# Optimization experiments

Hardware: AMD Instinct MI355X
Metric: run time of the kernel (lower is better)

Reference implementation:

```python
import jax, jax.numpy as jnp
import numpy as np

EPS = 1e-6
NUM_HEADS = 16

def _ln(x):
    # LayerNorm32, no affine, eps=1e-6, computed in fp32
    x32 = x.astype(jnp.float32)
    mu = jnp.mean(x32, axis=-1, keepdims=True)
    var = jnp.var(x32, axis=-1, keepdims=True)
    return ((x32 - mu) * jax.lax.rsqrt(var + EPS)).astype(x.dtype)

def _mha(q, k, v):
    # q,k,v: [B, L, H, D]
    d = q.shape[-1]
    scale = 1.0 / jnp.sqrt(jnp.asarray(d, q.dtype))
    s = jnp.einsum('bqhd,bkhd->bhqk', q, k) * scale
    p = jax.nn.softmax(s, axis=-1)
    o = jnp.einsum('bhqk,bkhd->bqhd', p, v)
    return o.reshape(o.shape[0], o.shape[1], -1)

def setup_inputs() -> dict:
    key = jax.random.key(0)
    ks = jax.random.split(key, 10)
    B, L, C, Lc, Cc = 4, 2048, 1024, 1024, 1024
    Dff = 4 * C
    s = 0.02
    return {
        'x': jax.random.normal(ks[0], (B, L, C), jnp.float32),
        'context': jax.random.normal(ks[1], (B, Lc, Cc), jnp.float32),
        'w_qkv': jax.random.normal(ks[2], (C, 3 * C), jnp.float32) * s,
        'b_qkv': jnp.zeros((3 * C,), jnp.float32),
        'w_os': jax.random.normal(ks[3], (C, C), jnp.float32) * s,
        'b_os': jnp.zeros((C,), jnp.float32),
        'w_qc': jax.random.normal(ks[4], (C, C), jnp.float32) * s,
        'b_qc': jnp.zeros((C,), jnp.float32),
        'w_kvc': jax.random.normal(ks[5], (Cc, 2 * C), jnp.float32) * s,
        'b_kvc': jnp.zeros((2 * C,), jnp.float32),
        'w_oc': jax.random.normal(ks[6], (C, C), jnp.float32) * s,
        'b_oc': jnp.zeros((C,), jnp.float32),
        'w_fc1': jax.random.normal(ks[7], (C, Dff), jnp.float32) * s,
        'b_fc1': jnp.zeros((Dff,), jnp.float32),
        'w_fc2': jax.random.normal(ks[8], (Dff, C), jnp.float32) * s,
        'b_fc2': jnp.zeros((C,), jnp.float32),
    }

def reference(x, context, w_qkv, b_qkv, w_os, b_os, w_qc, b_qc, w_kvc, b_kvc,
              w_oc, b_oc, w_fc1, b_fc1, w_fc2, b_fc2):
    B, L, C = x.shape
    H = NUM_HEADS
    D = C // H
    # --- self attention (pre-norm, full) ---
    h = _ln(x)
    qkv = (h @ w_qkv + b_qkv).reshape(B, L, 3, H, D)
    q, k, v = qkv[:, :, 0], qkv[:, :, 1], qkv[:, :, 2]
    h = _mha(q, k, v) @ w_os + b_os
    x = x + h
    # --- cross attention ---
    h = _ln(x)
    q = (h @ w_qc + b_qc).reshape(B, L, H, D)
    Lc = context.shape[1]
    kv = (context @ w_kvc + b_kvc).reshape(B, Lc, 2, H, D)
    k, v = kv[:, :, 0], kv[:, :, 1]
    h = _mha(q, k, v) @ w_oc + b_oc
    x = x + h
    # --- sparse FFN (GELU tanh) ---
    h = _ln(x)
    h = jax.nn.gelu(h @ w_fc1 + b_fc1, approximate=True) @ w_fc2 + b_fc2
    return x + h
```

## Files before the change

kernel.cpp:

```cpp
#include <hip/hip_runtime.h>

typedef unsigned short ushort_t;
typedef __attribute__((ext_vector_type(8))) short short8;
typedef __attribute__((ext_vector_type(4))) float f32x4;
typedef __attribute__((ext_vector_type(4))) unsigned short ushort4v;

__device__ inline ushort_t f2bf(float f) {
    union { float f; unsigned u; } v; v.f = f;
    return (ushort_t)((v.u + 0x7FFFu + ((v.u >> 16) & 1u)) >> 16);
}
__device__ inline float bf2f(ushort_t u) {
    union { unsigned u; float f; } v; v.u = ((unsigned)u) << 16;
    return v.f;
}

__device__ inline void gld16(const ushort_t* g, ushort_t* l) {
    __builtin_amdgcn_global_load_lds(
        (const __attribute__((address_space(1))) unsigned int*)g,
        (__attribute__((address_space(3))) unsigned int*)l, 16, 0, 0);
}

__device__ inline int xcd_swz(int id, int nwg) {
    int q = nwg >> 3;
    return (id & 7) * q + (id >> 3);
}

__global__ void w_transpose_bf16(const float* __restrict__ w, ushort_t* __restrict__ out,
                                 int K, int N) {
    __shared__ float t[64][65];
    const int k0 = blockIdx.y * 64, n0 = blockIdx.x * 64;
    const int tid = threadIdx.x;
#pragma unroll
    for (int i = 0; i < 16; i++) {
        int idx = tid + i * 256;
        int r = idx >> 6, c = idx & 63;
        t[r][c] = w[(size_t)(k0 + r) * N + n0 + c];
    }
    __syncthreads();
#pragma unroll
    for (int i = 0; i < 16; i++) {
        int idx = tid + i * 256;
        int nr = idx >> 6, kc = idx & 63;
        out[(size_t)(n0 + nr) * K + k0 + kc] = f2bf(t[kc][nr]);
    }
}

__global__ void v_transpose(const ushort_t* __restrict__ V, int vStride, int rowsPerBatch,
                            ushort_t* __restrict__ Vt, int Lk) {
    __shared__ __align__(16) ushort_t t[64][72];
    const int bh = blockIdx.y, k0 = blockIdx.x * 64;
    const int b = bh >> 4, h = bh & 15;
    const int tid = threadIdx.x;
    const ushort_t* src = V + (size_t)(b * rowsPerBatch + k0) * vStride + h * 64;
#pragma unroll
    for (int i = 0; i < 2; i++) {
        int ch = tid + i * 256;
        int r = ch >> 3, c = (ch & 7) * 8;
        *(short8*)(&t[r][c]) = *(const short8*)(src + (size_t)r * vStride + c);
    }
    __syncthreads();
#pragma unroll
    for (int i = 0; i < 2; i++) {
        int ch = tid + i * 256;
        int d = ch >> 3, c = (ch & 7) * 8;
        short8 o;
#pragma unroll
        for (int j = 0; j < 8; j++) o[j] = (short)t[c + j][d];
        *(short8*)(Vt + ((size_t)bh * 64 + d) * Lk + k0 + c) = o;
    }
}

__global__ void f32_to_bf16_vec(const float* __restrict__ in, ushort_t* __restrict__ out, int n4) {
    int i = blockIdx.x * blockDim.x + threadIdx.x;
    if (i < n4) {
        float4 v = ((const float4*)in)[i];
        ushort4v o;
        o[0] = f2bf(v.x); o[1] = f2bf(v.y); o[2] = f2bf(v.z); o[3] = f2bf(v.w);
        ((ushort4v*)out)[i] = o;
    }
}

__global__ void ln_rows(const float* __restrict__ in, ushort_t* __restrict__ out) {
    __shared__ float s1[4], s2[4];
    const int row = blockIdx.x;
    const int tid = threadIdx.x;
    const float4 v = ((const float4*)(in + (size_t)row * 1024))[tid];
    float s  = v.x + v.y + v.z + v.w;
    float ss = v.x * v.x + v.y * v.y + v.z * v.z + v.w * v.w;
#pragma unroll
    for (int d = 32; d >= 1; d >>= 1) {
        s  += __shfl_down(s, d, 64);
        ss += __shfl_down(ss, d, 64);
    }
    if ((tid & 63) == 0) { s1[tid >> 6] = s; s2[tid >> 6] = ss; }
    __syncthreads();
    float sum = s1[0] + s1[1] + s1[2] + s1[3];
    float sqs = s2[0] + s2[1] + s2[2] + s2[3];
    float mu  = sum * (1.0f / 1024.0f);
    float var = sqs * (1.0f / 1024.0f) - mu * mu;
    float rs  = rsqrtf(var + 1e-6f);
    ushort4v o;
    o[0] = f2bf((v.x - mu) * rs);
    o[1] = f2bf((v.y - mu) * rs);
    o[2] = f2bf((v.z - mu) * rs);
    o[3] = f2bf((v.w - mu) * rs);
    ((ushort4v*)(out + (size_t)row * 1024))[tid] = o;
}

#define EPI_BF16 0
#define EPI_GELU 1
#define EPI_RES  2

template <int EPI>
__global__ void gemm_bt(const ushort_t* __restrict__ A, const ushort_t* __restrict__ Bt,
                        const float* __restrict__ bias, const float* __restrict__ res,
                        void* __restrict__ outp, int M, int N, int K) {
    __shared__ __align__(16) ushort_t As[128 * 64];
    __shared__ __align__(16) ushort_t Bs[128 * 64];
    const int tid = threadIdx.x;
    const int lane = tid & 63, wave = tid >> 6;
    const int nwg = gridDim.x * gridDim.y;
    const int sid = xcd_swz(blockIdx.y * gridDim.x + blockIdx.x, nwg);
    const int m0 = (sid / gridDim.x) * 128, n0 = (sid % gridDim.x) * 128;
    const int wr = (wave >> 1) * 64, wc = (wave & 1) * 64;
    const int lr = lane & 15, lg = lane >> 4;

    f32x4 acc[4][4];
#pragma unroll
    for (int i = 0; i < 4; i++)
#pragma unroll
        for (int j = 0; j < 4; j++) acc[i][j] = f32x4{0.f, 0.f, 0.f, 0.f};

    for (int k0 = 0; k0 < K; k0 += 64) {
#pragma unroll
        for (int i = 0; i < 4; i++) {
            int ch = tid + i * 256;
            int r = ch >> 3;
            int kcs = (((ch & 7) ^ (r & 7))) * 8;
            gld16(A  + (size_t)(m0 + r) * K + k0 + kcs, As + ch * 8);
            gld16(Bt + (size_t)(n0 + r) * K + k0 + kcs, Bs + ch * 8);
        }
        __syncthreads();
#pragma unroll
        for (int ks = 0; ks < 2; ks++) {
            short8 af[4], bfr[4];
#pragma unroll
            for (int m = 0; m < 4; m++) {
                int r = wr + m * 16 + lr;
                int kc = ks * 4 + lg;
                af[m] = *(const short8*)(As + r * 64 + ((kc ^ (r & 7)) << 3));
            }
#pragma unroll
            for (int n = 0; n < 4; n++) {
                int r = wc + n * 16 + lr;
                int kc = ks * 4 + lg;
                bfr[n] = *(const short8*)(Bs + r * 64 + ((kc ^ (r & 7)) << 3));
            }
#pragma unroll
            for (int m = 0; m < 4; m++)
#pragma unroll
                for (int n = 0; n < 4; n++)
                    acc[m][n] = __builtin_amdgcn_mfma_f32_16x16x32_bf16(af[m], bfr[n], acc[m][n], 0, 0, 0);
        }
        __syncthreads();
    }

#pragma unroll
    for (int m = 0; m < 4; m++) {
        int rowb = m0 + wr + m * 16 + lg * 4;
#pragma unroll
        for (int n = 0; n < 4; n++) {
            int col = n0 + wc + n * 16 + lr;
            float bcol = bias[col];
            f32x4 v = acc[m][n];
#pragma unroll
            for (int q = 0; q < 4; q++) {
                float x = v[q] + bcol;
                if (EPI == EPI_GELU) {
                    float u = 0.7978845608028654f * (x + 0.044715f * x * x * x);
                    x = 0.5f * x * (1.0f + tanhf(u));
                }
                size_t off = (size_t)(rowb + q) * N + col;
                if (EPI == EPI_RES) ((float*)outp)[off] = x + res[off];
                else                ((ushort_t*)outp)[off] = f2bf(x);
            }
        }
    }
}

__global__ __launch_bounds__(512, 2)
void attn_fwd(const ushort_t* __restrict__ Q, int qStride,
              const ushort_t* __restrict__ Kp, int kvStride, int kvBatchRows,
              const ushort_t* __restrict__ Vt, int Lk,
              ushort_t* __restrict__ O) {
    __shared__ __align__(16) ushort_t Ks[2][64 * 64];
    __shared__ __align__(16) ushort_t Vts[2][64 * 64];
    __shared__ __align__(16) ushort_t Ps[8][16 * 64];
    const int tid = threadIdx.x, lane = tid & 63, wave = tid >> 6;
    const int lr = lane & 15, lg = lane >> 4;
    const int sid = xcd_swz(blockIdx.x, gridDim.x);
    const int qb = sid & 15, h = (sid >> 4) & 15, b = sid >> 8;
    const int qRow0 = b * 2048 + qb * 128;
    const int kvRow0 = b * kvBatchRows;
    const int hc = h * 64;
    const ushort_t* vt_base = Vt + (size_t)(b * 16 + h) * 64 * Lk;

    short8 qf[2];
    {
        const ushort_t* qrow = Q + (size_t)(qRow0 + wave * 16 + lr) * qStride + hc;
        short8 r0 = *(const short8*)(qrow + lg * 8);
        short8 r1 = *(const short8*)(qrow + 32 + lg * 8);
#pragma unroll
        for (int j = 0; j < 8; j++) {
            qf[0][j] = (short)f2bf(bf2f((ushort_t)r0[j]) * 0.125f);
            qf[1][j] = (short)f2bf(bf2f((ushort_t)r1[j]) * 0.125f);
        }
    }

    f32x4 oacc[4];
#pragma unroll
    for (int d = 0; d < 4; d++) oacc[d] = f32x4{0.f, 0.f, 0.f, 0.f};
    float mrun = -INFINITY, lrun = 0.f;

    const int nt = Lk >> 6;

    auto stage = [&](int buf, int kt) {
        int r = tid >> 3;
        int kcs = (((tid & 7) ^ (r & 7))) * 8;
        gld16(Kp + (size_t)(kvRow0 + kt + r) * kvStride + hc + kcs, Ks[buf] + tid * 8);
        gld16(vt_base + (size_t)r * Lk + kt + kcs, Vts[buf] + tid * 8);
    };

    stage(0, 0);
    __syncthreads();
    int cur = 0;

    for (int t = 0; t < nt; ++t) {
        if (t + 1 < nt) stage(cur ^ 1, (t + 1) * 64);

        const ushort_t* Kc = Ks[cur];
        const ushort_t* Vc = Vts[cur];

        f32x4 sacc[4];
        __builtin_amdgcn_s_setprio(1);
#pragma unroll
        for (int n = 0; n < 4; n++) {
            int r = n * 16 + lr;
            short8 k0 = *(const short8*)(Kc + r * 64 + ((lg ^ (r & 7)) << 3));
            short8 k1 = *(const short8*)(Kc + r * 64 + (((4 + lg) ^ (r & 7)) << 3));
            f32x4 s = f32x4{0.f, 0.f, 0.f, 0.f};
            s = __builtin_amdgcn_mfma_f32_16x16x32_bf16(k0, qf[0], s, 0, 0, 0);
            s = __builtin_amdgcn_mfma_f32_16x16x32_bf16(k1, qf[1], s, 0, 0, 0);
            sacc[n] = s;
        }
        __builtin_amdgcn_s_setprio(0);

        float mx = sacc[0][0];
#pragma unroll
        for (int n = 0; n < 4; n++)
#pragma unroll
            for (int r = 0; r < 4; r++) if (n | r) mx = fmaxf(mx, sacc[n][r]);
        mx = fmaxf(mx, __shfl_xor(mx, 16, 64));
        mx = fmaxf(mx, __shfl_xor(mx, 32, 64));

        if (!__all(mx <= mrun + 8.0f)) {
            float mnew = fmaxf(mrun, mx);
            float al = __expf(mrun - mnew);
            float a0 = __shfl(al, lg * 4 + 0, 64);
            float a1 = __shfl(al, lg * 4 + 1, 64);
            float a2 = __shfl(al, lg * 4 + 2, 64);
            float a3 = __shfl(al, lg * 4 + 3, 64);
#pragma unroll
            for (int dn = 0; dn < 4; dn++) {
                oacc[dn][0] *= a0; oacc[dn][1] *= a1;
                oacc[dn][2] *= a2; oacc[dn][3] *= a3;
            }
            lrun *= al;
            mrun = mnew;
        }

        float rsum = 0.f;
#pragma unroll
        for (int n = 0; n < 4; n++)
#pragma unroll
            for (int r = 0; r < 4; r++) {
                float p = __expf(sacc[n][r] - mrun);
                sacc[n][r] = p;
                rsum += p;
            }
        rsum += __shfl_xor(rsum, 16, 64);
        rsum += __shfl_xor(rsum, 32, 64);
        lrun += rsum;

        ushort_t* Pw = &Ps[wave][0];
#pragma unroll
        for (int n = 0; n < 4; n++) {
            unsigned w0, w1;
            asm("v_cvt_pk_bf16_f32 %0, %1, %2" : "=v"(w0) : "v"(sacc[n][0]), "v"(sacc[n][1]));
            asm("v_cvt_pk_bf16_f32 %0, %1, %2" : "=v"(w1) : "v"(sacc[n][2]), "v"(sacc[n][3]));
            int kc = n * 2 + (lg >> 1);
            uint2 u; u.x = w0; u.y = w1;
            *(uint2*)((char*)Pw + lr * 128 + ((kc ^ (lr & 7)) << 4) + (lg & 1) * 8) = u;
        }

        short8 pf0 = *(const short8*)(Pw + lr * 64 + ((lg ^ (lr & 7)) << 3));
        short8 pf1 = *(const short8*)(Pw + lr * 64 + (((4 + lg) ^ (lr & 7)) << 3));
        __builtin_amdgcn_s_setprio(1);
#pragma unroll
        for (int dn = 0; dn < 4; dn++) {
            int r = dn * 16 + lr;
            short8 v0 = *(const short8*)(Vc + r * 64 + ((lg ^ (r & 7)) << 3));
            short8 v1 = *(const short8*)(Vc + r * 64 + (((4 + lg) ^ (r & 7)) << 3));
            oacc[dn] = __builtin_amdgcn_mfma_f32_16x16x32_bf16(pf0, v0, oacc[dn], 0, 0, 0);
            oacc[dn] = __builtin_amdgcn_mfma_f32_16x16x32_bf16(pf1, v1, oacc[dn], 0, 0, 0);
        }
        __builtin_amdgcn_s_setprio(0);
        __syncthreads();
        cur ^= 1;
    }

    float linv[4];
#pragma unroll
    for (int r = 0; r < 4; r++) linv[r] = 1.0f / __shfl(lrun, lg * 4 + r, 64);

#pragma unroll
    for (int dn = 0; dn < 4; dn++)
#pragma unroll
        for (int q = 0; q < 4; q++) {
            float o = oacc[dn][q] * linv[q];
            int row = qRow0 + wave * 16 + lg * 4 + q;
            int col = hc + dn * 16 + lr;
            O[(size_t)row * 1024 + col] = f2bf(o);
        }
}

extern "C" void kernel_launch(void* const* d_in, const int* in_sizes, int n_in,
                              void* d_out, int out_size, void* d_ws, size_t ws_size,
                              hipStream_t stream) {
    const float* x     = (const float*)d_in[0];
    const float* ctx   = (const float*)d_in[1];
    const float* w_qkv = (const float*)d_in[2];
    const float* b_qkv = (const float*)d_in[3];
    const float* w_os  = (const float*)d_in[4];
    const float* b_os  = (const float*)d_in[5];
    const float* w_qc  = (const float*)d_in[6];
    const float* b_qc  = (const float*)d_in[7];
    const float* w_kvc = (const float*)d_in[8];
    const float* b_kvc = (const float*)d_in[9];
    const float* w_oc  = (const float*)d_in[10];
    const float* b_oc  = (const float*)d_in[11];
    const float* w_fc1 = (const float*)d_in[12];
    const float* b_fc1 = (const float*)d_in[13];
    const float* w_fc2 = (const float*)d_in[14];
    const float* b_fc2 = (const float*)d_in[15];
    float* out = (float*)d_out;

    char* ws = (char*)d_ws;
    ushort_t* wqkvT = (ushort_t*)(ws + 0);
    ushort_t* wosT  = (ushort_t*)(ws + 6291456);
    ushort_t* wqcT  = (ushort_t*)(ws + 8388608);
    ushort_t* wkvcT = (ushort_t*)(ws + 10485760);
    ushort_t* wocT  = (ushort_t*)(ws + 14680064);
    ushort_t* wfc1T = (ushort_t*)(ws + 16777216);
    ushort_t* wfc2T = (ushort_t*)(ws + 25165824);
    ushort_t* qkv_bf  = (ushort_t*)(ws + 33554432);
    ushort_t* q_bf    = (ushort_t*)(ws + 33554432);
    ushort_t* kv_bf   = (ushort_t*)(ws + 50331648);
    ushort_t* vt_c    = (ushort_t*)(ws + 67108864);
    ushort_t* ffn_bf  = (ushort_t*)(ws + 33554432);
    ushort_t* ctx_bf  = (ushort_t*)(ws + 83886080);
    ushort_t* attn_bf = (ushort_t*)(ws + 92274688);
    ushort_t* h_bf    = (ushort_t*)(ws + 109051904);
    ushort_t* vt_s    = (ushort_t*)(ws + 109051904);

    const dim3 tb(256);
    const dim3 tb512(512);
    w_transpose_bf16<<<dim3(48, 16), tb, 0, stream>>>(w_qkv, wqkvT, 1024, 3072);
    w_transpose_bf16<<<dim3(16, 16), tb, 0, stream>>>(w_os,  wosT,  1024, 1024);
    w_transpose_bf16<<<dim3(16, 16), tb, 0, stream>>>(w_qc,  wqcT,  1024, 1024);
    w_transpose_bf16<<<dim3(32, 16), tb, 0, stream>>>(w_kvc, wkvcT, 1024, 2048);
    w_transpose_bf16<<<dim3(16, 16), tb, 0, stream>>>(w_oc,  wocT,  1024, 1024);
    w_transpose_bf16<<<dim3(64, 16), tb, 0, stream>>>(w_fc1, wfc1T, 1024, 4096);
    w_transpose_bf16<<<dim3(16, 64), tb, 0, stream>>>(w_fc2, wfc2T, 4096, 1024);
    f32_to_bf16_vec<<<4096, tb, 0, stream>>>(ctx, ctx_bf, 1048576);

    ln_rows<<<8192, tb, 0, stream>>>(x, h_bf);
    gemm_bt<EPI_BF16><<<dim3(24, 64), tb, 0, stream>>>(h_bf, wqkvT, b_qkv, nullptr, qkv_bf, 8192, 3072, 1024);
    v_transpose<<<dim3(32, 64), tb, 0, stream>>>(qkv_bf + 2048, 3072, 2048, vt_s, 2048);
    attn_fwd<<<dim3(1024), tb512, 0, stream>>>(qkv_bf, 3072, qkv_bf + 1024, 3072, 2048,
                                               vt_s, 2048, attn_bf);
    gemm_bt<EPI_RES><<<dim3(8, 64), tb, 0, stream>>>(attn_bf, wosT, b_os, x, out, 8192, 1024, 1024);

    ln_rows<<<8192, tb, 0, stream>>>(out, h_bf);
    gemm_bt<EPI_BF16><<<dim3(8, 64), tb, 0, stream>>>(h_bf, wqcT, b_qc, nullptr, q_bf, 8192, 1024, 1024);
    gemm_bt<EPI_BF16><<<dim3(16, 32), tb, 0, stream>>>(ctx_bf, wkvcT, b_kvc, nullptr, kv_bf, 4096, 2048, 1024);
    v_transpose<<<dim3(16, 64), tb, 0, stream>>>(kv_bf + 1024, 2048, 1024, vt_c, 1024);
    attn_fwd<<<dim3(1024), tb512, 0, stream>>>(q_bf, 1024, kv_bf, 2048, 1024,
                                               vt_c, 1024, attn_bf);
    gemm_bt<EPI_RES><<<dim3(8, 64), tb, 0, stream>>>(attn_bf, wocT, b_oc, out, out, 8192, 1024, 1024);

    ln_rows<<<8192, tb, 0, stream>>>(out, h_bf);
    gemm_bt<EPI_GELU><<<dim3(32, 64), tb, 0, stream>>>(h_bf, wfc1T, b_fc1, nullptr, ffn_bf, 8192, 4096, 1024);
    gemm_bt<EPI_RES><<<dim3(8, 64), tb, 0, stream>>>(ffn_bf, wfc2T, b_fc2, out, out, 8192, 1024, 4096);
}
```

Baseline: 589.6 us.

## Rework attention to 32x32x16 MFMA with register P exchange and exp2 softmax

The attention kernel moves from 16x16x32 MFMA tiles with 8 waves of 16 query rows to 32x32x16 MFMA tiles with 4 waves of 32 query rows each. Each lane now holds a full query row, so the row max and sum need only one cross-lane shuffle. The P tile is passed to the PV MFMA through a lane-xor-32 shuffle in registers instead of an LDS round trip, and softmax uses exp2 with log2(e) folded into the Q scale, with the running max preloaded into the S accumulators. Block size drops to 256 threads with a launch bound of 3 blocks per CU. The larger tiles use more registers per lane, which may limit occupancy, and the loads per tile are split into two passes.

New measurement: 600.7 us. No clear change (+1.9%).

```diff
diff --git a/kernel.cpp b/kernel.cpp
--- a/kernel.cpp
+++ b/kernel.cpp
@@ -3,6 +3,7 @@
 typedef unsigned short ushort_t;
 typedef __attribute__((ext_vector_type(8))) short short8;
 typedef __attribute__((ext_vector_type(4))) float f32x4;
+typedef __attribute__((ext_vector_type(16))) float f32x16;
 typedef __attribute__((ext_vector_type(4))) unsigned short ushort4v;
 
 __device__ inline ushort_t f2bf(float f) {
@@ -188,47 +189,52 @@
     }
 }
 
-__global__ __launch_bounds__(512, 2)
+__global__ __launch_bounds__(256, 3)
 void attn_fwd(const ushort_t* __restrict__ Q, int qStride,
               const ushort_t* __restrict__ Kp, int kvStride, int kvBatchRows,
               const ushort_t* __restrict__ Vt, int Lk,
               ushort_t* __restrict__ O) {
     __shared__ __align__(16) ushort_t Ks[2][64 * 64];
     __shared__ __align__(16) ushort_t Vts[2][64 * 64];
-    __shared__ __align__(16) ushort_t Ps[8][16 * 64];
     const int tid = threadIdx.x, lane = tid & 63, wave = tid >> 6;
-    const int lr = lane & 15, lg = lane >> 4;
+    const int ql = lane & 31;
+    const int hh = lane >> 5;
     const int sid = xcd_swz(blockIdx.x, gridDim.x);
-    const int qb = sid & 15, h = (sid >> 4) & 15, b = sid >> 8;
+    const int qb = sid & 15, hd = (sid >> 4) & 15, b = sid >> 8;
     const int qRow0 = b * 2048 + qb * 128;
     const int kvRow0 = b * kvBatchRows;
-    const int hc = h * 64;
-    const ushort_t* vt_base = Vt + (size_t)(b * 16 + h) * 64 * Lk;
-
-    short8 qf[2];
+    const int hc = hd * 64;
+    const ushort_t* vt_base = Vt + (size_t)(b * 16 + hd) * 64 * Lk;
+
+    short8 qf[4];
     {
-        const ushort_t* qrow = Q + (size_t)(qRow0 + wave * 16 + lr) * qStride + hc;
-        short8 r0 = *(const short8*)(qrow + lg * 8);
-        short8 r1 = *(const short8*)(qrow + 32 + lg * 8);
-#pragma unroll
-        for (int j = 0; j < 8; j++) {
-            qf[0][j] = (short)f2bf(bf2f((ushort_t)r0[j]) * 0.125f);
-            qf[1][j] = (short)f2bf(bf2f((ushort_t)r1[j]) * 0.125f);
-        }
-    }
-
-    f32x4 oacc[4];
-#pragma unroll
-    for (int d = 0; d < 4; d++) oacc[d] = f32x4{0.f, 0.f, 0.f, 0.f};
-    float mrun = -INFINITY, lrun = 0.f;
+        const ushort_t* qrow = Q + (size_t)(qRow0 + wave * 32 + ql) * qStride + hc + hh * 8;
+        const float s = 0.125f * 1.44269504088896f;
+#pragma unroll
+        for (int mi = 0; mi < 4; mi++) {
+            short8 r = *(const short8*)(qrow + mi * 16);
+#pragma unroll
+            for (int j = 0; j < 8; j++) qf[mi][j] = (short)f2bf(bf2f((ushort_t)r[j]) * s);
+        }
+    }
+
+    f32x16 o0, o1;
+#pragma unroll
+    for (int r = 0; r < 16; r++) { o0[r] = 0.f; o1[r] = 0.f; }
+    float mrun = 0.f, lrun = 0.f;
 
     const int nt = Lk >> 6;
+    const int sw = ql & 7;
 
     auto stage = [&](int buf, int kt) {
-        int r = tid >> 3;
-        int kcs = (((tid & 7) ^ (r & 7))) * 8;
-        gld16(Kp + (size_t)(kvRow0 + kt + r) * kvStride + hc + kcs, Ks[buf] + tid * 8);
-        gld16(vt_base + (size_t)r * Lk + kt + kcs, Vts[buf] + tid * 8);
+#pragma unroll
+        for (int i = 0; i < 2; i++) {
+            int ch = tid + i * 256;
+            int r = ch >> 3;
+            int kcs = (((ch & 7) ^ (r & 7))) * 8;
+            gld16(Kp + (size_t)(kvRow0 + kt + r) * kvStride + hc + kcs, Ks[buf] + ch * 8);
+            gld16(vt_base + (size_t)r * Lk + kt + kcs, Vts[buf] + ch * 8);
+        }
     };
 
     stage(0, 0);
@@ -241,97 +247,91 @@
         const ushort_t* Kc = Ks[cur];
         const ushort_t* Vc = Vts[cur];
 
-        f32x4 sacc[4];
+        f32x16 s0, s1;
+#pragma unroll
+        for (int r = 0; r < 16; r++) { s0[r] = -mrun; s1[r] = -mrun; }
         __builtin_amdgcn_s_setprio(1);
 #pragma unroll
-        for (int n = 0; n < 4; n++) {
-            int r = n * 16 + lr;
-            short8 k0 = *(const short8*)(Kc + r * 64 + ((lg ^ (r & 7)) << 3));
-            short8 k1 = *(const short8*)(Kc + r * 64 + (((4 + lg) ^ (r & 7)) << 3));
-            f32x4 s = f32x4{0.f, 0.f, 0.f, 0.f};
-            s = __builtin_amdgcn_mfma_f32_16x16x32_bf16(k0, qf[0], s, 0, 0, 0);
-            s = __builtin_amdgcn_mfma_f32_16x16x32_bf16(k1, qf[1], s, 0, 0, 0);
-            sacc[n] = s;
+        for (int mi = 0; mi < 4; mi++) {
+            short8 a0 = *(const short8*)(Kc + ql * 64 + (((2 * mi + hh) ^ sw) << 3));
+            short8 a1 = *(const short8*)(Kc + (32 + ql) * 64 + (((2 * mi + hh) ^ sw) << 3));
+            s0 = __builtin_amdgcn_mfma_f32_32x32x16_bf16(a0, qf[mi], s0, 0, 0, 0);
+            s1 = __builtin_amdgcn_mfma_f32_32x32x16_bf16(a1, qf[mi], s1, 0, 0, 0);
         }
         __builtin_amdgcn_s_setprio(0);
 
-        float mx = sacc[0][0];
-#pragma unroll
-        for (int n = 0; n < 4; n++)
-#pragma unroll
-            for (int r = 0; r < 4; r++) if (n | r) mx = fmaxf(mx, sacc[n][r]);
-        mx = fmaxf(mx, __shfl_xor(mx, 16, 64));
+        float mx = fmaxf(s0[0], s0[1]);
+#pragma unroll
+        for (int r = 2; r < 16; r++) mx = fmaxf(mx, s0[r]);
+#pragma unroll
+        for (int r = 0; r < 16; r++) mx = fmaxf(mx, s1[r]);
         mx = fmaxf(mx, __shfl_xor(mx, 32, 64));
 
-        if (!__all(mx <= mrun + 8.0f)) {
-            float mnew = fmaxf(mrun, mx);
-            float al = __expf(mrun - mnew);
-            float a0 = __shfl(al, lg * 4 + 0, 64);
-            float a1 = __shfl(al, lg * 4 + 1, 64);
-            float a2 = __shfl(al, lg * 4 + 2, 64);
-            float a3 = __shfl(al, lg * 4 + 3, 64);
-#pragma unroll
-            for (int dn = 0; dn < 4; dn++) {
-                oacc[dn][0] *= a0; oacc[dn][1] *= a1;
-                oacc[dn][2] *= a2; oacc[dn][3] *= a3;
-            }
+        if (!__all(mx <= 8.0f)) {
+            float d = fmaxf(mx, 0.0f);
+            float al = exp2f(-d);
+#pragma unroll
+            for (int r = 0; r < 16; r++) { o0[r] *= al; o1[r] *= al; }
             lrun *= al;
-            mrun = mnew;
+            mrun += d;
+#pragma unroll
+            for (int r = 0; r < 16; r++) { s0[r] -= d; s1[r] -= d; }
         }
 
         float rsum = 0.f;
 #pragma unroll
-        for (int n = 0; n < 4; n++)
-#pragma unroll
-            for (int r = 0; r < 4; r++) {
-                float p = __expf(sacc[n][r] - mrun);
-                sacc[n][r] = p;
-                rsum += p;
-            }
-        rsum += __shfl_xor(rsum, 16, 64);
+        for (int r = 0; r < 16; r++) { s0[r] = exp2f(s0[r]); rsum += s0[r]; }
+#pragma unroll
+        for (int r = 0; r < 16; r++) { s1[r] = exp2f(s1[r]); rsum += s1[r]; }
         rsum += __shfl_xor(rsum, 32, 64);
         lrun += rsum;
 
-        ushort_t* Pw = &Ps[wave][0];
-#pragma unroll
-        for (int n = 0; n < 4; n++) {
-            unsigned w0, w1;
-            asm("v_cvt_pk_bf16_f32 %0, %1, %2" : "=v"(w0) : "v"(sacc[n][0]), "v"(sacc[n][1]));
-            asm("v_cvt_pk_bf16_f32 %0, %1, %2" : "=v"(w1) : "v"(sacc[n][2]), "v"(sacc[n][3]));
-            int kc = n * 2 + (lg >> 1);
-            uint2 u; u.x = w0; u.y = w1;
-            *(uint2*)((char*)Pw + lr * 128 + ((kc ^ (lr & 7)) << 4) + (lg & 1) * 8) = u;
-        }
-
-        short8 pf0 = *(const short8*)(Pw + lr * 64 + ((lg ^ (lr & 7)) << 3));
-        short8 pf1 = *(const short8*)(Pw + lr * 64 + (((4 + lg) ^ (lr & 7)) << 3));
+        unsigned W0[8], W1[8];
+#pragma unroll
+        for (int g = 0; g < 4; g++) {
+            asm("v_cvt_pk_bf16_f32 %0, %1, %2" : "=v"(W0[g * 2 + 0]) : "v"(s0[4 * g + 0]), "v"(s0[4 * g + 1]));
+            asm("v_cvt_pk_bf16_f32 %0, %1, %2" : "=v"(W0[g * 2 + 1]) : "v"(s0[4 * g + 2]), "v"(s0[4 * g + 3]));
+            asm("v_cvt_pk_bf16_f32 %0, %1, %2" : "=v"(W1[g * 2 + 0]) : "v"(s1[4 * g + 0]), "v"(s1[4 * g + 1]));
+            asm("v_cvt_pk_bf16_f32 %0, %1, %2" : "=v"(W1[g * 2 + 1]) : "v"(s1[4 * g + 2]), "v"(s1[4 * g + 3]));
+        }
+
         __builtin_amdgcn_s_setprio(1);
 #pragma unroll
-        for (int dn = 0; dn < 4; dn++) {
-            int r = dn * 16 + lr;
-            short8 v0 = *(const short8*)(Vc + r * 64 + ((lg ^ (r & 7)) << 3));
-            short8 v1 = *(const short8*)(Vc + r * 64 + (((4 + lg) ^ (r & 7)) << 3));
-            oacc[dn] = __builtin_amdgcn_mfma_f32_16x16x32_bf16(pf0, v0, oacc[dn], 0, 0, 0);
-            oacc[dn] = __builtin_amdgcn_mfma_f32_16x16x32_bf16(pf1, v1, oacc[dn], 0, 0, 0);
+        for (int w = 0; w < 4; w++) {
+            const int p2 = (w & 1) * 2;
+            union { unsigned u[4]; short8 s8; } pf;
+#pragma unroll
+            for (int i = 0; i < 2; i++) {
+                unsigned A0 = (w >> 1) ? W1[p2 * 2 + i] : W0[p2 * 2 + i];
+                unsigned A1 = (w >> 1) ? W1[(p2 + 1) * 2 + i] : W0[(p2 + 1) * 2 + i];
+                unsigned own  = hh ? A1 : A0;
+                unsigned send = hh ? A0 : A1;
+                unsigned recv = __shfl_xor(send, 32, 64);
+                pf.u[0 + i] = hh ? recv : own;
+                pf.u[2 + i] = hh ? own : recv;
+            }
+            short8 v0 = *(const short8*)(Vc + ql * 64 + (((2 * w + hh) ^ sw) << 3));
+            short8 v1 = *(const short8*)(Vc + (32 + ql) * 64 + (((2 * w + hh) ^ sw) << 3));
+            o0 = __builtin_amdgcn_mfma_f32_32x32x16_bf16(v0, pf.s8, o0, 0, 0, 0);
+            o1 = __builtin_amdgcn_mfma_f32_32x32x16_bf16(v1, pf.s8, o1, 0, 0, 0);
         }
         __builtin_amdgcn_s_setprio(0);
         __syncthreads();
         cur ^= 1;
     }
 
-    float linv[4];
-#pragma unroll
-    for (int r = 0; r < 4; r++) linv[r] = 1.0f / __shfl(lrun, lg * 4 + r, 64);
-
-#pragma unroll
-    for (int dn = 0; dn < 4; dn++)
-#pragma unroll
-        for (int q = 0; q < 4; q++) {
-            float o = oacc[dn][q] * linv[q];
-            int row = qRow0 + wave * 16 + lg * 4 + q;
-            int col = hc + dn * 16 + lr;
-            O[(size_t)row * 1024 + col] = f2bf(o);
-        }
+    float linv = 1.0f / lrun;
+    ushort_t* orow = O + (size_t)(qRow0 + wave * 32 + ql) * 1024 + hc + 4 * hh;
+#pragma unroll
+    for (int g = 0; g < 4; g++) {
+        ushort4v ov;
+#pragma unroll
+        for (int j = 0; j < 4; j++) ov[j] = f2bf(o0[4 * g + j] * linv);
+        *(ushort4v*)(orow + 8 * g) = ov;
+#pragma unroll
+        for (int j = 0; j < 4; j++) ov[j] = f2bf(o1[4 * g + j] * linv);
+        *(ushort4v*)(orow + 32 + 8 * g) = ov;
+    }
 }
 
 extern "C" void kernel_launch(void* const* d_in, const int* in_sizes, int n_in,
@@ -374,7 +374,6 @@
     ushort_t* vt_s    = (ushort_t*)(ws + 109051904);
 
     const dim3 tb(256);
-    const dim3 tb512(512);
     w_transpose_bf16<<<dim3(48, 16), tb, 0, stream>>>(w_qkv, wqkvT, 1024, 3072);
     w_transpose_bf16<<<dim3(16, 16), tb, 0, stream>>>(w_os,  wosT,  1024, 1024);
     w_transpose_bf16<<<dim3(16, 16), tb, 0, stream>>>(w_qc,  wqcT,  1024, 1024);
@@ -387,16 +386,16 @@
     ln_rows<<<8192, tb, 0, stream>>>(x, h_bf);
     gemm_bt<EPI_BF16><<<dim3(24, 64), tb, 0, stream>>>(h_bf, wqkvT, b_qkv, nullptr, qkv_bf, 8192, 3072, 1024);
     v_transpose<<<dim3(32, 64), tb, 0, stream>>>(qkv_bf + 2048, 3072, 2048, vt_s, 2048);
-    attn_fwd<<<dim3(1024), tb512, 0, stream>>>(qkv_bf, 3072, qkv_bf + 1024, 3072, 2048,
-                                               vt_s, 2048, attn_bf);
+    attn_fwd<<<dim3(1024), tb, 0, stream>>>(qkv_bf, 3072, qkv_bf + 1024, 3072, 2048,
+                                            vt_s, 2048, attn_bf);
     gemm_bt<EPI_RES><<<dim3(8, 64), tb, 0, stream>>>(attn_bf, wosT, b_os, x, out, 8192, 1024, 1024);
 
     ln_rows<<<8192, tb, 0, stream>>>(out, h_bf);
     gemm_bt<EPI_BF16><<<dim3(8, 64), tb, 0, stream>>>(h_bf, wqcT, b_qc, nullptr, q_bf, 8192, 1024, 1024);
     gemm_bt<EPI_BF16><<<dim3(16, 32), tb, 0, stream>>>(ctx_bf, wkvcT, b_kvc, nullptr, kv_bf, 4096, 2048, 1024);
     v_transpose<<<dim3(16, 64), tb, 0, stream>>>(kv_bf + 1024, 2048, 1024, vt_c, 1024);
-    attn_fwd<<<dim3(1024), tb512, 0, stream>>>(q_bf, 1024, kv_bf, 2048, 1024,
-                                               vt_c, 1024, attn_bf);
+    attn_fwd<<<dim3(1024), tb, 0, stream>>>(q_bf, 1024, kv_bf, 2048, 1024,
+                                            vt_c, 1024, attn_bf);
     gemm_bt<EPI_RES><<<dim3(8, 64), tb, 0, stream>>>(attn_bf, wocT, b_oc, out, out, 8192, 1024, 1024);
 
     ln_rows<<<8192, tb, 0, stream>>>(out, h_bf);
```

## Add 256x256-tile GEMM with phased prefetch for QKV and FC1 projections

Applied to the files above, without the earlier changes.

Adds a new GEMM kernel with 256x256 output tiles, 512 threads and a double-buffered LDS pipeline. Global loads for the next k-tiles are interleaved across four MFMA phases, with explicit waitcnt and barriers between them. It replaces the 128-tile GEMM for the two widest projections (QKV and FC1) to raise arithmetic intensity and cut global traffic per FLOP. The cost is much higher register and LDS use (128 KB of shared buffers), fewer blocks in the grid, and hand-tuned vmcnt counts that must match the issued loads.

New measurement: 611.4 us. +3.7%, slower.

```diff
diff --git a/kernel.cpp b/kernel.cpp
--- a/kernel.cpp
+++ b/kernel.cpp
@@ -183,6 +183,128 @@
                 size_t off = (size_t)(rowb + q) * N + col;
                 if (EPI == EPI_RES) ((float*)outp)[off] = x + res[off];
                 else                ((ushort_t*)outp)[off] = f2bf(x);
+            }
+        }
+    }
+}
+
+template <int EPI>
+__global__ __launch_bounds__(512, 2)
+void gemm256_bt(const ushort_t* __restrict__ A, const ushort_t* __restrict__ Bt,
+                const float* __restrict__ bias,
+                void* __restrict__ outp, int M, int N, int K) {
+    __shared__ __align__(16) ushort_t As[2][256 * 64];
+    __shared__ __align__(16) ushort_t Bs[2][256 * 64];
+    const int tid = threadIdx.x;
+    const int lane = tid & 63, wave = tid >> 6;
+    const int wm = wave >> 2, wn = wave & 3;
+    const int lr = lane & 15, lg = lane >> 4;
+    const int ntx = gridDim.x;
+    const int sid = xcd_swz(blockIdx.y * ntx + blockIdx.x, ntx * gridDim.y);
+    const int m0 = (sid / ntx) * 256, n0 = (sid % ntx) * 256;
+    const int nkt = K >> 6;
+
+    f32x4 acc[8][4];
+#pragma unroll
+    for (int i = 0; i < 8; i++)
+#pragma unroll
+        for (int j = 0; j < 4; j++) acc[i][j] = f32x4{0.f, 0.f, 0.f, 0.f};
+
+    auto stageAQ = [&](int slot, int kt, int q) {
+        int r_ = (tid >> 8) * 128 + q * 32 + ((tid >> 3) & 31);
+        int c_ = tid & 7;
+        gld16(A + (size_t)(m0 + r_) * K + kt + ((c_ ^ (r_ & 7)) << 3),
+              &As[slot][r_ * 64 + c_ * 8]);
+    };
+    auto stageBH = [&](int slot, int kt, int h) {
+#pragma unroll
+        for (int i = 0; i < 2; i++) {
+            int ch = tid + i * 512;
+            int r_ = h * 128 + (ch >> 3);
+            int c_ = ch & 7;
+            gld16(Bt + (size_t)(n0 + r_) * K + kt + ((c_ ^ (r_ & 7)) << 3),
+                  &Bs[slot][r_ * 64 + c_ * 8]);
+        }
+    };
+
+#define RD_A(slot, mf, ks)                                                      \
+    (*(const short8*)(&As[slot][(wm * 128 + (mf) * 16 + lr) * 64 +              \
+        ((((ks) * 4 + lg) ^ ((wm * 128 + (mf) * 16 + lr) & 7)) << 3)]))
+#define RD_B(slot, nf, ks)                                                      \
+    (*(const short8*)(&Bs[slot][(wn * 64 + (nf) * 16 + lr) * 64 +               \
+        ((((ks) * 4 + lg) ^ ((wn * 64 + (nf) * 16 + lr) & 7)) << 3)]))
+
+#define GPHASE(P, STAGE_STMT)                                                   \
+    {                                                                           \
+        short8 a0 = RD_A(s, 2 * (P), 0),     a1 = RD_A(s, 2 * (P), 1);          \
+        short8 a2 = RD_A(s, 2 * (P) + 1, 0), a3 = RD_A(s, 2 * (P) + 1, 1);      \
+        STAGE_STMT;                                                             \
+        __builtin_amdgcn_s_barrier();                                           \
+        asm volatile("s_waitcnt lgkmcnt(0)" ::: "memory");                      \
+        __builtin_amdgcn_sched_barrier(0);                                      \
+        __builtin_amdgcn_s_setprio(1);                                          \
+        _Pragma("unroll")                                                       \
+        for (int nf = 0; nf < 4; nf++) {                                        \
+            acc[2 * (P)][nf]     = __builtin_amdgcn_mfma_f32_16x16x32_bf16(     \
+                a0, bfr[nf][0], acc[2 * (P)][nf], 0, 0, 0);                     \
+            acc[2 * (P)][nf]     = __builtin_amdgcn_mfma_f32_16x16x32_bf16(     \
+                a1, bfr[nf][1], acc[2 * (P)][nf], 0, 0, 0);                     \
+            acc[2 * (P) + 1][nf] = __builtin_amdgcn_mfma_f32_16x16x32_bf16(     \
+                a2, bfr[nf][0], acc[2 * (P) + 1][nf], 0, 0, 0);                 \
+            acc[2 * (P) + 1][nf] = __builtin_amdgcn_mfma_f32_16x16x32_bf16(     \
+                a3, bfr[nf][1], acc[2 * (P) + 1][nf], 0, 0, 0);                 \
+        }                                                                       \
+        __builtin_amdgcn_s_setprio(0);                                          \
+        if (more2) asm volatile("s_waitcnt vmcnt(8)" ::: "memory");             \
+        else       asm volatile("s_waitcnt vmcnt(0)" ::: "memory");             \
+        __builtin_amdgcn_s_barrier();                                           \
+        __builtin_amdgcn_sched_barrier(0);                                      \
+    }
+
+    stageBH(0, 0, 0); stageBH(0, 0, 1);
+    stageAQ(0, 0, 0); stageAQ(0, 0, 1); stageAQ(0, 0, 2); stageAQ(0, 0, 3);
+    stageBH(1, 64, 0); stageBH(1, 64, 1);
+    stageAQ(1, 64, 0); stageAQ(1, 64, 1);
+    asm volatile("s_waitcnt vmcnt(0)" ::: "memory");
+    __builtin_amdgcn_s_barrier();
+    __builtin_amdgcn_sched_barrier(0);
+
+    int s = 0;
+    for (int t = 0; t < nkt; ++t, s ^= 1) {
+        short8 bfr[4][2];
+#pragma unroll
+        for (int nf = 0; nf < 4; nf++) {
+            bfr[nf][0] = RD_B(s, nf, 0);
+            bfr[nf][1] = RD_B(s, nf, 1);
+        }
+        const bool more2 = (t + 2 < nkt);
+        GPHASE(0, { if (t + 1 < nkt) { stageAQ(s ^ 1, (t + 1) << 6, 2);
+                                       stageAQ(s ^ 1, (t + 1) << 6, 3); } })
+        GPHASE(1, { if (more2) stageBH(s, (t + 2) << 6, 0); })
+        GPHASE(2, { if (more2) stageBH(s, (t + 2) << 6, 1); })
+        GPHASE(3, { if (more2) { stageAQ(s, (t + 2) << 6, 0);
+                                 stageAQ(s, (t + 2) << 6, 1); } })
+    }
+#undef GPHASE
+#undef RD_A
+#undef RD_B
+
+#pragma unroll
+    for (int mf = 0; mf < 8; mf++) {
+        int rowb = m0 + wm * 128 + mf * 16 + lg * 4;
+#pragma unroll
+        for (int nf = 0; nf < 4; nf++) {
+            int col = n0 + wn * 64 + nf * 16 + lr;
+            float bcol = bias[col];
+            f32x4 v = acc[mf][nf];
+#pragma unroll
+            for (int q = 0; q < 4; q++) {
+                float x = v[q] + bcol;
+                if (EPI == EPI_GELU) {
+                    float u = 0.7978845608028654f * (x + 0.044715f * x * x * x);
+                    x = 0.5f * x * (1.0f + tanhf(u));
+                }
+                ((ushort_t*)outp)[(size_t)(rowb + q) * N + col] = f2bf(x);
             }
         }
     }
@@ -385,7 +507,7 @@
     f32_to_bf16_vec<<<4096, tb, 0, stream>>>(ctx, ctx_bf, 1048576);
 
     ln_rows<<<8192, tb, 0, stream>>>(x, h_bf);
-    gemm_bt<EPI_BF16><<<dim3(24, 64), tb, 0, stream>>>(h_bf, wqkvT, b_qkv, nullptr, qkv_bf, 8192, 3072, 1024);
+    gemm256_bt<EPI_BF16><<<dim3(12, 32), tb512, 0, stream>>>(h_bf, wqkvT, b_qkv, qkv_bf, 8192, 3072, 1024);
     v_transpose<<<dim3(32, 64), tb, 0, stream>>>(qkv_bf + 2048, 3072, 2048, vt_s, 2048);
     attn_fwd<<<dim3(1024), tb512, 0, stream>>>(qkv_bf, 3072, qkv_bf + 1024, 3072, 2048,
                                                vt_s, 2048, attn_bf);
@@ -400,6 +522,6 @@
     gemm_bt<EPI_RES><<<dim3(8, 64), tb, 0, stream>>>(attn_bf, wocT, b_oc, out, out, 8192, 1024, 1024);
 
     ln_rows<<<8192, tb, 0, stream>>>(out, h_bf);
-    gemm_bt<EPI_GELU><<<dim3(32, 64), tb, 0, stream>>>(h_bf, wfc1T, b_fc1, nullptr, ffn_bf, 8192, 4096, 1024);
+    gemm256_bt<EPI_GELU><<<dim3(16, 32), tb512, 0, stream>>>(h_bf, wfc1T, b_fc1, ffn_bf, 8192, 4096, 1024);
     gemm_bt<EPI_RES><<<dim3(8, 64), tb, 0, stream>>>(ffn_bf, wfc2T, b_fc2, out, out, 8192, 1024, 4096);
 }
```
